# Kernel tuning notes

Measured on AMD Instinct MI355X. Metric: run time of the kernel, lower is better.

## Reference

```python
import jax, jax.numpy as jnp
import numpy as np

B, D, L, H = 8, 512, 2048, 8
DH = D // H
NEG = -1e30


def setup_inputs() -> dict:
    key = jax.random.key(0)
    k1, k2, k3, k4 = jax.random.split(key, 4)
    queries = jax.random.normal(k1, (B, D, L), dtype=jnp.float32)
    mask = jax.random.randint(k2, (B, L), 0, 2, dtype=jnp.int32)
    w_mem = jax.random.normal(k3, (2 * D, D), dtype=jnp.float32) * (1.0 / np.sqrt(D))
    w_q = jax.random.normal(k4, (D, D), dtype=jnp.float32) * (1.0 / np.sqrt(D))
    return {"queries": queries, "mask": mask, "w_mem": w_mem, "w_q": w_q}


def reference(queries, mask, w_mem, w_q):
    # 1x1 conv == pointwise GEMM over channel dim. queries: [B, D, L]
    memory = jnp.einsum('od,bdl->blo', w_mem, queries)  # [B, L, 2D]
    query = jnp.einsum('od,bdl->blo', w_q, queries)     # [B, L, D]

    def split_heads(x):  # [B, L, C] -> [B, H, L, C/H]
        b, l, c = x.shape
        return x.reshape(b, l, H, c // H).transpose(0, 2, 1, 3)

    k, v = memory[..., :D], memory[..., D:]
    Q = split_heads(query) * (DH ** -0.5)  # [B, H, L, DH]
    K = split_heads(k)
    V = split_heads(v)

    logits = jnp.einsum('bhqd,bhkd->bhqk', Q, K)  # [B, H, L, L]
    m = mask.astype(jnp.float32)[:, None, None, :]  # [B, 1, 1, L]
    logits = logits * m + (1.0 - m) * NEG
    weights = jax.nn.softmax(logits, axis=-1)
    x = jnp.einsum('bhqk,bhkd->bhqd', weights, V)  # [B, H, L, DH]
    # combine heads -> [B, L, D] -> transpose back to [B, D, L]
    out = x.transpose(0, 2, 1, 3).reshape(B, L, D).transpose(0, 2, 1)
    return out
```

## Files before the change

### kernel.cpp

```cpp
#include <hip/hip_runtime.h>
#include <hip/hip_bf16.h>

#define NB 8
#define ND 512
#define NL 2048
#define NH 8
#define NDH 64
#define VROWS 72

typedef __attribute__((ext_vector_type(8))) short bf16x8;
typedef __attribute__((ext_vector_type(4))) float f32x4;
typedef __attribute__((ext_vector_type(4))) unsigned int u32x4;

__device__ __forceinline__ unsigned short f2bf(float x) {
    return (unsigned short)((__float_as_uint(x) + 0x8000u) >> 16);
}

__device__ __forceinline__ float exp2_fast(float x) {
#if __has_builtin(__builtin_amdgcn_exp2f)
    return __builtin_amdgcn_exp2f(x);
#else
    return exp2f(x);
#endif
}

__device__ __forceinline__ unsigned int pack_bf16(float a, float b) {
    unsigned int ua = __float_as_uint(a) + 0x8000u;
    unsigned int ub = __float_as_uint(b) + 0x8000u;
    return __builtin_amdgcn_perm(ub, ua, 0x07060302u);
}

__device__ __forceinline__ void async16(void* lds, const void* g) {
    __builtin_amdgcn_global_load_lds(
        (const __attribute__((address_space(1))) unsigned int*)g,
        (__attribute__((address_space(3))) unsigned int*)lds, 16, 0, 0);
}

__global__ __launch_bounds__(256) void convert_w(
    const float* __restrict__ w_mem, const float* __restrict__ w_q,
    unsigned short* __restrict__ Wc)
{
    int idx = (blockIdx.x * 256 + threadIdx.x) * 8;
    int o = idx >> 9, k = idx & 511;
    const float* src;
    float sc;
    if (o < 1024) { src = w_mem + (size_t)o * ND + k; sc = 1.0f; }
    else          { src = w_q + (size_t)(o - 1024) * ND + k;
                    sc = 0.125f * 1.4426950408889634f; }
    float4 f0 = *(const float4*)src;
    float4 f1 = *(const float4*)(src + 4);
    ushort4 p0 = { f2bf(f0.x * sc), f2bf(f0.y * sc), f2bf(f0.z * sc), f2bf(f0.w * sc) };
    ushort4 p1 = { f2bf(f1.x * sc), f2bf(f1.y * sc), f2bf(f1.z * sc), f2bf(f1.w * sc) };
    *(ushort4*)(Wc + idx) = p0;
    *(ushort4*)(Wc + idx + 4) = p1;
}

__global__ __launch_bounds__(256) void convert_xt(
    const float* __restrict__ qin, unsigned short* __restrict__ Xt)
{
    __shared__ __align__(16) unsigned short T[64][72];
    const int b = blockIdx.z, d0 = blockIdx.y * 64, l0 = blockIdx.x * 64;
    const int t = threadIdx.x;
    const float* X = qin + ((size_t)b * ND + d0) * NL + l0;
    #pragma unroll
    for (int i = 0; i < 4; ++i) {
        int e = t + i * 256;
        int d = e >> 4, l4 = (e & 15) * 4;
        float4 v = *(const float4*)(X + (size_t)d * NL + l4);
        T[l4 + 0][d] = f2bf(v.x);
        T[l4 + 1][d] = f2bf(v.y);
        T[l4 + 2][d] = f2bf(v.z);
        T[l4 + 3][d] = f2bf(v.w);
    }
    __syncthreads();
    #pragma unroll
    for (int i = 0; i < 2; ++i) {
        int e = t + i * 256;
        int row = e >> 3, c8 = (e & 7) * 8;
        *(bf16x8*)(Xt + ((size_t)b * NL + l0 + row) * ND + d0 + c8) =
            *(const bf16x8*)&T[row][c8];
    }
}

__global__ __launch_bounds__(256) void write_vmask(
    const int* __restrict__ maskp, unsigned short* __restrict__ Vt)
{
    const int bh = blockIdx.x;
    const int b = bh >> 3;
    unsigned short* base = Vt + (size_t)bh * VROWS * NL;
    unsigned short* row64 = base + (size_t)64 * NL;
    for (int kk = threadIdx.x; kk < NL; kk += 256) {
        int s  = (kk & 32) | ((kk & 12) << 1) | ((kk & 16) >> 2) | (kk & 3);
        int lp = (kk & ~63) | s;
        row64[lp] = maskp[b * NL + kk] ? (unsigned short)0x3F80 : (unsigned short)0;
    }
    unsigned short* z = base + (size_t)65 * NL;
    for (int i = threadIdx.x; i < 7 * NL; i += 256) z[i] = 0;
}

__global__ __launch_bounds__(256, 3) void proj_mfma(
    const unsigned short* __restrict__ Wc,
    const unsigned short* __restrict__ Xt,
    const int* __restrict__ maskp,
    unsigned short* __restrict__ Kh,
    unsigned short* __restrict__ Qh,
    unsigned short* __restrict__ Vt)
{
    __shared__ __align__(16) unsigned short As[128 * 64];
    __shared__ __align__(16) unsigned short Bs[128 * 64];

    const int b  = blockIdx.z;
    const int m0 = blockIdx.y * 128;
    const int n0 = blockIdx.x * 128;
    const int t  = threadIdx.x;
    const int w = t >> 6, lane = t & 63, quad = lane >> 4, lq = lane & 15;
    const int wo = (w >> 1) * 64, wl = (w & 1) * 64;
    const int lr = lane >> 3;
    const int cbsw = (lane & 7) ^ lr;

    f32x4 acc[4][4];
    #pragma unroll
    for (int im = 0; im < 4; ++im)
        #pragma unroll
        for (int in = 0; in < 4; ++in)
            acc[im][in] = (f32x4){0.f, 0.f, 0.f, 0.f};

    for (int k0 = 0; k0 < ND; k0 += 64) {
        __syncthreads();
        #pragma unroll 2
        for (int i = w; i < 32; i += 4) {
            if (i < 16) {
                int R = i * 8;
                async16(&As[R * 64],
                        Wc + (size_t)(m0 + R + lr) * ND + k0 + cbsw * 8);
            } else {
                int R = (i - 16) * 8;
                async16(&Bs[R * 64],
                        Xt + ((size_t)b * NL + n0 + R + lr) * ND + k0 + cbsw * 8);
            }
        }
        __syncthreads();

        #pragma unroll
        for (int ks = 0; ks < 2; ++ks) {
            bf16x8 af[4], bfr[4];
            #pragma unroll
            for (int im = 0; im < 4; ++im) {
                int r = wo + im * 16 + lq;
                af[im] = *(const bf16x8*)&As[r * 64 + (((ks * 4 + quad) ^ (lq & 7)) * 8)];
            }
            #pragma unroll
            for (int in = 0; in < 4; ++in) {
                int r = wl + in * 16 + lq;
                bfr[in] = *(const bf16x8*)&Bs[r * 64 + (((ks * 4 + quad) ^ (lq & 7)) * 8)];
            }
            #pragma unroll
            for (int im = 0; im < 4; ++im)
                #pragma unroll
                for (int in = 0; in < 4; ++in)
                    acc[im][in] = __builtin_amdgcn_mfma_f32_16x16x32_bf16(
                        af[im], bfr[in], acc[im][in], 0, 0, 0);
        }
    }

    const int reg = (m0 + wo) >> 9;
    if (reg != 1) {
        unsigned short* dst = (reg == 0) ? Kh : Qh;
        #pragma unroll
        for (int im = 0; im < 4; ++im) {
            int o  = (m0 + wo + im * 16 + quad * 4) & 511;
            int hh = o >> 6, dh = o & 63;
            #pragma unroll
            for (int in = 0; in < 4; ++in) {
                int l = n0 + wl + in * 16 + lq;
                ushort4 pk = { f2bf(acc[im][in][0]), f2bf(acc[im][in][1]),
                               f2bf(acc[im][in][2]), f2bf(acc[im][in][3]) };
                *(ushort4*)&dst[(((size_t)b * NH + hh) * NL + l) * NDH + dh] = pk;
            }
        }
    } else {
        float mv[4];
        #pragma unroll
        for (int in = 0; in < 4; ++in)
            mv[in] = (float)maskp[b * NL + (n0 + wl + in * 16 + lq)];
        #pragma unroll
        for (int im = 0; im < 4; ++im) {
            int o  = (m0 + wo + im * 16 + quad * 4) & 511;
            int hh = o >> 6, dh = o & 63;
            #pragma unroll
            for (int in = 0; in < 4; ++in) {
                int l  = n0 + wl + in * 16 + lq;
                int kk = l & 63;
                int s  = (kk & 32) | ((kk & 12) << 1) | ((kk & 16) >> 2) | (kk & 3);
                int lp = (l & ~63) | s;
                #pragma unroll
                for (int r = 0; r < 4; ++r)
                    Vt[(((size_t)(b * NH + hh)) * VROWS + dh + r) * NL + lp] =
                        f2bf(acc[im][in][r] * mv[in]);
            }
        }
    }
}

__global__ __launch_bounds__(256, 2) void attn_mfma(
    const unsigned short* __restrict__ Qh,
    const unsigned short* __restrict__ Kh,
    const unsigned short* __restrict__ Vt,
    float* __restrict__ out)
{
    __shared__ __align__(16) unsigned short Ks2[2][64 * 64];
    __shared__ __align__(16) unsigned short Vs2[2][80 * 64];

    const int id = blockIdx.x;
    const int h  = id & 7;
    const int b  = (id >> 3) & 7;
    const int q0 = (id >> 6) * 256;
    const int t = threadIdx.x;
    const int w = t >> 6, lane = t & 63, quad = lane >> 4, lq = lane & 15;
    const int lr = lane >> 3;
    const int cbsw = (lane & 7) ^ lr;

    const unsigned short* Qg = Qh + ((size_t)(b * NH + h)) * NL * NDH;
    const unsigned short* Kg = Kh + ((size_t)(b * NH + h)) * NL * NDH;
    const unsigned short* Vg = Vt + ((size_t)(b * NH + h)) * VROWS * NL;

    #pragma unroll 2
    for (int i = w; i < 17; i += 4) {
        if (i < 8) {
            int R = i * 8;
            async16(&Ks2[0][R * 64], Kg + (size_t)(R + lr) * NDH + cbsw * 8);
        } else {
            int R = (i - 8) * 8;
            async16(&Vs2[0][R * 64], Vg + (size_t)(R + lr) * NL + cbsw * 8);
        }
    }

    bf16x8 qf[4][2];
    #pragma unroll
    for (int ni = 0; ni < 4; ++ni)
        #pragma unroll
        for (int ks = 0; ks < 2; ++ks)
            qf[ni][ks] = *(const bf16x8*)
                &Qg[(size_t)(q0 + w * 64 + ni * 16 + lq) * NDH + ks * 32 + quad * 8];

    f32x4 oacc[5][4];
    #pragma unroll
    for (int dm = 0; dm < 5; ++dm)
        #pragma unroll
        for (int ni = 0; ni < 4; ++ni)
            oacc[dm][ni] = (f32x4){0.f, 0.f, 0.f, 0.f};

    int cur = 0;
    for (int k0 = 0; k0 < NL; k0 += 64) {
        __syncthreads();

        if (k0 + 64 < NL) {
            const int kn = k0 + 64, nb = cur ^ 1;
            #pragma unroll 2
            for (int i = w; i < 17; i += 4) {
                if (i < 8) {
                    int R = i * 8;
                    async16(&Ks2[nb][R * 64],
                            Kg + (size_t)(kn + R + lr) * NDH + cbsw * 8);
                } else {
                    int R = (i - 8) * 8;
                    async16(&Vs2[nb][R * 64],
                            Vg + (size_t)(R + lr) * NL + kn + cbsw * 8);
                }
            }
        }

        const unsigned short* KsB = Ks2[cur];
        const unsigned short* VsB = Vs2[cur];

        f32x4 sacc[4][4];
        #pragma unroll
        for (int mi = 0; mi < 4; ++mi)
            #pragma unroll
            for (int ni = 0; ni < 4; ++ni)
                sacc[mi][ni] = (f32x4){0.f, 0.f, 0.f, 0.f};
        #pragma unroll
        for (int ks = 0; ks < 2; ++ks) {
            bf16x8 kf[4];
            #pragma unroll
            for (int mi = 0; mi < 4; ++mi)
                kf[mi] = *(const bf16x8*)
                    &KsB[(mi * 16 + lq) * 64 + (((ks * 4 + quad) ^ (lq & 7)) * 8)];
            #pragma unroll
            for (int mi = 0; mi < 4; ++mi)
                #pragma unroll
                for (int ni = 0; ni < 4; ++ni)
                    sacc[mi][ni] = __builtin_amdgcn_mfma_f32_16x16x32_bf16(
                        kf[mi], qf[ni][ks], sacc[mi][ni], 0, 0, 0);
        }

        u32x4 pfu[4][2];
        #pragma unroll
        for (int mi = 0; mi < 4; ++mi) {
            const int ks = mi >> 1, jp = (mi & 1) * 2;
            #pragma unroll
            for (int ni = 0; ni < 4; ++ni) {
                float e0 = exp2_fast(sacc[mi][ni][0]);
                float e1 = exp2_fast(sacc[mi][ni][1]);
                float e2 = exp2_fast(sacc[mi][ni][2]);
                float e3 = exp2_fast(sacc[mi][ni][3]);
                pfu[ni][ks][jp + 0] = pack_bf16(e0, e1);
                pfu[ni][ks][jp + 1] = pack_bf16(e2, e3);
            }
        }

        #pragma unroll
        for (int ks = 0; ks < 2; ++ks) {
            bf16x8 vf[5];
            #pragma unroll
            for (int dm = 0; dm < 5; ++dm)
                vf[dm] = *(const bf16x8*)
                    &VsB[(dm * 16 + lq) * 64 + (((ks * 4 + quad) ^ (lq & 7)) * 8)];
            #pragma unroll
            for (int dm = 0; dm < 5; ++dm)
                #pragma unroll
                for (int ni = 0; ni < 4; ++ni)
                    oacc[dm][ni] = __builtin_amdgcn_mfma_f32_16x16x32_bf16(
                        vf[dm], __builtin_bit_cast(bf16x8, pfu[ni][ks]),
                        oacc[dm][ni], 0, 0, 0);
        }
        cur ^= 1;
    }

    float inv[4];
    #pragma unroll
    for (int ni = 0; ni < 4; ++ni)
        inv[ni] = 1.0f / __shfl(oacc[4][ni][0], lq);

    #pragma unroll
    for (int dm = 0; dm < 4; ++dm)
        #pragma unroll
        for (int ni = 0; ni < 4; ++ni)
            #pragma unroll
            for (int r = 0; r < 4; ++r) {
                int dh = dm * 16 + quad * 4 + r;
                int l  = q0 + w * 64 + ni * 16 + lq;
                out[((size_t)b * ND + h * NDH + dh) * NL + l] =
                    oacc[dm][ni][r] * inv[ni];
            }
}

extern "C" void kernel_launch(void* const* d_in, const int* in_sizes, int n_in,
                              void* d_out, int out_size, void* d_ws, size_t ws_size,
                              hipStream_t stream) {
    const float* queries = (const float*)d_in[0];
    const int*   maskp   = (const int*)d_in[1];
    const float* w_mem   = (const float*)d_in[2];
    const float* w_q     = (const float*)d_in[3];
    float* out = (float*)d_out;

    const size_t headElems  = (size_t)NB * NH * NL * NDH;
    const size_t vElems     = (size_t)NB * NH * VROWS * NL;
    unsigned short* Kh = (unsigned short*)d_ws;
    unsigned short* Vt = Kh + headElems;
    unsigned short* Qh = Vt + vElems;
    unsigned short* Wc = Qh + headElems;
    unsigned short* Xt = Wc + (size_t)1536 * ND;

    convert_w<<<384, 256, 0, stream>>>(w_mem, w_q, Wc);

    dim3 gx(NL / 64, ND / 64, NB);
    convert_xt<<<gx, 256, 0, stream>>>(queries, Xt);

    write_vmask<<<NB * NH, 256, 0, stream>>>(maskp, Vt);

    dim3 g1(NL / 128, 1536 / 128, NB);
    proj_mfma<<<g1, 256, 0, stream>>>(Wc, Xt, maskp, Kh, Qh, Vt);

    attn_mfma<<<512, 256, 0, stream>>>(Qh, Kh, Vt, out);
}
```

Before: 204.6 us.

## Swap V-projection MFMA operands for vector stores, merge prep kernels, unroll attention loop

For the V rows of the projection, the MFMA operands are swapped so each lane holds four consecutive sequence positions. This lets the masked V tile be written with packed ushort4 stores, and the mask read as int4, instead of scattered 2-byte stores. The weight-conversion and V-mask-row kernels are merged into one launch, and the zeroing of the V padding rows 65-71 is dropped. The attention loop is unrolled by two with fixed double-buffer pointers, and the score accumulator starts from zero inside the first MFMA. The unzeroed padding rows feed MFMAs whose outputs are never stored, so correctness depends on that.

After: 225.0 us. +10.0%, slower.

```diff
diff --git a/kernel.cpp b/kernel.cpp
--- a/kernel.cpp
+++ b/kernel.cpp
@@ -36,23 +36,36 @@
         (__attribute__((address_space(3))) unsigned int*)lds, 16, 0, 0);
 }
 
-__global__ __launch_bounds__(256) void convert_w(
+__global__ __launch_bounds__(256) void prep_small(
     const float* __restrict__ w_mem, const float* __restrict__ w_q,
-    unsigned short* __restrict__ Wc)
+    const int* __restrict__ maskp,
+    unsigned short* __restrict__ Wc, unsigned short* __restrict__ Vt)
 {
-    int idx = (blockIdx.x * 256 + threadIdx.x) * 8;
-    int o = idx >> 9, k = idx & 511;
-    const float* src;
-    float sc;
-    if (o < 1024) { src = w_mem + (size_t)o * ND + k; sc = 1.0f; }
-    else          { src = w_q + (size_t)(o - 1024) * ND + k;
-                    sc = 0.125f * 1.4426950408889634f; }
-    float4 f0 = *(const float4*)src;
-    float4 f1 = *(const float4*)(src + 4);
-    ushort4 p0 = { f2bf(f0.x * sc), f2bf(f0.y * sc), f2bf(f0.z * sc), f2bf(f0.w * sc) };
-    ushort4 p1 = { f2bf(f1.x * sc), f2bf(f1.y * sc), f2bf(f1.z * sc), f2bf(f1.w * sc) };
-    *(ushort4*)(Wc + idx) = p0;
-    *(ushort4*)(Wc + idx + 4) = p1;
+    const int bid = blockIdx.x;
+    if (bid < 384) {
+        int idx = (bid * 256 + threadIdx.x) * 8;
+        int o = idx >> 9, k = idx & 511;
+        const float* src;
+        float sc;
+        if (o < 1024) { src = w_mem + (size_t)o * ND + k; sc = 1.0f; }
+        else          { src = w_q + (size_t)(o - 1024) * ND + k;
+                        sc = 0.125f * 1.4426950408889634f; }
+        float4 f0 = *(const float4*)src;
+        float4 f1 = *(const float4*)(src + 4);
+        ushort4 p0 = { f2bf(f0.x * sc), f2bf(f0.y * sc), f2bf(f0.z * sc), f2bf(f0.w * sc) };
+        ushort4 p1 = { f2bf(f1.x * sc), f2bf(f1.y * sc), f2bf(f1.z * sc), f2bf(f1.w * sc) };
+        *(ushort4*)(Wc + idx) = p0;
+        *(ushort4*)(Wc + idx + 4) = p1;
+    } else {
+        const int bh = bid - 384;
+        const int b = bh >> 3;
+        unsigned short* row64 = Vt + ((size_t)bh * VROWS + 64) * NL;
+        for (int kk = threadIdx.x; kk < NL; kk += 256) {
+            int s = (kk & 32) | ((kk & 12) << 1) | ((kk & 16) >> 2) | (kk & 3);
+            row64[(kk & ~63) | s] =
+                maskp[b * NL + kk] ? (unsigned short)0x3F80 : (unsigned short)0;
+        }
+    }
 }
 
 __global__ __launch_bounds__(256) void convert_xt(
@@ -80,22 +93,6 @@
         *(bf16x8*)(Xt + ((size_t)b * NL + l0 + row) * ND + d0 + c8) =
             *(const bf16x8*)&T[row][c8];
     }
-}
-
-__global__ __launch_bounds__(256) void write_vmask(
-    const int* __restrict__ maskp, unsigned short* __restrict__ Vt)
-{
-    const int bh = blockIdx.x;
-    const int b = bh >> 3;
-    unsigned short* base = Vt + (size_t)bh * VROWS * NL;
-    unsigned short* row64 = base + (size_t)64 * NL;
-    for (int kk = threadIdx.x; kk < NL; kk += 256) {
-        int s  = (kk & 32) | ((kk & 12) << 1) | ((kk & 16) >> 2) | (kk & 3);
-        int lp = (kk & ~63) | s;
-        row64[lp] = maskp[b * NL + kk] ? (unsigned short)0x3F80 : (unsigned short)0;
-    }
-    unsigned short* z = base + (size_t)65 * NL;
-    for (int i = threadIdx.x; i < 7 * NL; i += 256) z[i] = 0;
 }
 
 __global__ __launch_bounds__(256, 3) void proj_mfma(
@@ -117,13 +114,16 @@
     const int wo = (w >> 1) * 64, wl = (w & 1) * 64;
     const int lr = lane >> 3;
     const int cbsw = (lane & 7) ^ lr;
+    const bool isV = (m0 >= 512) && (m0 < 1024);
+    const f32x4 z4 = {0.f, 0.f, 0.f, 0.f};
 
     f32x4 acc[4][4];
     #pragma unroll
     for (int im = 0; im < 4; ++im)
         #pragma unroll
-        for (int in = 0; in < 4; ++in)
-            acc[im][in] = (f32x4){0.f, 0.f, 0.f, 0.f};
+        for (int in = 0; in < 4; ++in) acc[im][in] = z4;
+
+    const int sw[2] = {(quad ^ (lq & 7)) * 8, ((4 + quad) ^ (lq & 7)) * 8};
 
     for (int k0 = 0; k0 < ND; k0 += 64) {
         __syncthreads();
@@ -145,27 +145,31 @@
         for (int ks = 0; ks < 2; ++ks) {
             bf16x8 af[4], bfr[4];
             #pragma unroll
-            for (int im = 0; im < 4; ++im) {
-                int r = wo + im * 16 + lq;
-                af[im] = *(const bf16x8*)&As[r * 64 + (((ks * 4 + quad) ^ (lq & 7)) * 8)];
-            }
-            #pragma unroll
-            for (int in = 0; in < 4; ++in) {
-                int r = wl + in * 16 + lq;
-                bfr[in] = *(const bf16x8*)&Bs[r * 64 + (((ks * 4 + quad) ^ (lq & 7)) * 8)];
-            }
-            #pragma unroll
             for (int im = 0; im < 4; ++im)
-                #pragma unroll
-                for (int in = 0; in < 4; ++in)
-                    acc[im][in] = __builtin_amdgcn_mfma_f32_16x16x32_bf16(
-                        af[im], bfr[in], acc[im][in], 0, 0, 0);
-        }
-    }
-
-    const int reg = (m0 + wo) >> 9;
-    if (reg != 1) {
-        unsigned short* dst = (reg == 0) ? Kh : Qh;
+                af[im] = *(const bf16x8*)&As[(wo + im * 16 + lq) * 64 + sw[ks]];
+            #pragma unroll
+            for (int in = 0; in < 4; ++in)
+                bfr[in] = *(const bf16x8*)&Bs[(wl + in * 16 + lq) * 64 + sw[ks]];
+            if (!isV) {
+                #pragma unroll
+                for (int im = 0; im < 4; ++im)
+                    #pragma unroll
+                    for (int in = 0; in < 4; ++in)
+                        acc[im][in] = __builtin_amdgcn_mfma_f32_16x16x32_bf16(
+                            af[im], bfr[in], acc[im][in], 0, 0, 0);
+            } else {
+                #pragma unroll
+                for (int im = 0; im < 4; ++im)
+                    #pragma unroll
+                    for (int in = 0; in < 4; ++in)
+                        acc[im][in] = __builtin_amdgcn_mfma_f32_16x16x32_bf16(
+                            bfr[im], af[in], acc[im][in], 0, 0, 0);
+            }
+        }
+    }
+
+    if (!isV) {
+        unsigned short* dst = (m0 < 512) ? Kh : Qh;
         #pragma unroll
         for (int im = 0; im < 4; ++im) {
             int o  = (m0 + wo + im * 16 + quad * 4) & 511;
@@ -179,24 +183,23 @@
             }
         }
     } else {
-        float mv[4];
-        #pragma unroll
-        for (int in = 0; in < 4; ++in)
-            mv[in] = (float)maskp[b * NL + (n0 + wl + in * 16 + lq)];
         #pragma unroll
         for (int im = 0; im < 4; ++im) {
-            int o  = (m0 + wo + im * 16 + quad * 4) & 511;
-            int hh = o >> 6, dh = o & 63;
+            int l4 = n0 + wl + im * 16 + quad * 4;
+            int kk = l4 & 63;
+            int s4 = (kk & 32) | ((kk & 12) << 1) | ((kk & 16) >> 2);
+            int lp = (l4 & ~63) | s4;
+            int4 m4 = *(const int4*)&maskp[b * NL + l4];
+            float mv[4] = {(float)m4.x, (float)m4.y, (float)m4.z, (float)m4.w};
             #pragma unroll
             for (int in = 0; in < 4; ++in) {
-                int l  = n0 + wl + in * 16 + lq;
-                int kk = l & 63;
-                int s  = (kk & 32) | ((kk & 12) << 1) | ((kk & 16) >> 2) | (kk & 3);
-                int lp = (l & ~63) | s;
-                #pragma unroll
-                for (int r = 0; r < 4; ++r)
-                    Vt[(((size_t)(b * NH + hh)) * VROWS + dh + r) * NL + lp] =
-                        f2bf(acc[im][in][r] * mv[in]);
+                int o  = m0 - 512 + wo + in * 16 + lq;
+                int hh = o >> 6, dd = o & 63;
+                ushort4 pk = { f2bf(acc[im][in][0] * mv[0]),
+                               f2bf(acc[im][in][1] * mv[1]),
+                               f2bf(acc[im][in][2] * mv[2]),
+                               f2bf(acc[im][in][3] * mv[3]) };
+                *(ushort4*)&Vt[(((size_t)(b * NH + hh)) * VROWS + dd) * NL + lp] = pk;
             }
         }
     }
@@ -219,21 +222,28 @@
     const int w = t >> 6, lane = t & 63, quad = lane >> 4, lq = lane & 15;
     const int lr = lane >> 3;
     const int cbsw = (lane & 7) ^ lr;
+    const f32x4 z4 = {0.f, 0.f, 0.f, 0.f};
 
     const unsigned short* Qg = Qh + ((size_t)(b * NH + h)) * NL * NDH;
     const unsigned short* Kg = Kh + ((size_t)(b * NH + h)) * NL * NDH;
     const unsigned short* Vg = Vt + ((size_t)(b * NH + h)) * VROWS * NL;
 
-    #pragma unroll 2
-    for (int i = w; i < 17; i += 4) {
-        if (i < 8) {
-            int R = i * 8;
-            async16(&Ks2[0][R * 64], Kg + (size_t)(R + lr) * NDH + cbsw * 8);
-        } else {
-            int R = (i - 8) * 8;
-            async16(&Vs2[0][R * 64], Vg + (size_t)(R + lr) * NL + cbsw * 8);
-        }
-    }
+    const int sw[2] = {(quad ^ (lq & 7)) * 8, ((4 + quad) ^ (lq & 7)) * 8};
+
+    auto stage = [&](unsigned short* Kd, unsigned short* Vd, int kn) {
+        #pragma unroll 2
+        for (int i = w; i < 17; i += 4) {
+            if (i < 8) {
+                int R = i * 8;
+                async16(Kd + R * 64, Kg + (size_t)(kn + R + lr) * NDH + cbsw * 8);
+            } else {
+                int R = (i - 8) * 8;
+                async16(Vd + R * 64, Vg + (size_t)(R + lr) * NL + kn + cbsw * 8);
+            }
+        }
+    };
+
+    stage(Ks2[0], Vs2[0], 0);
 
     bf16x8 qf[4][2];
     #pragma unroll
@@ -247,51 +257,35 @@
     #pragma unroll
     for (int dm = 0; dm < 5; ++dm)
         #pragma unroll
-        for (int ni = 0; ni < 4; ++ni)
-            oacc[dm][ni] = (f32x4){0.f, 0.f, 0.f, 0.f};
-
-    int cur = 0;
-    for (int k0 = 0; k0 < NL; k0 += 64) {
+        for (int ni = 0; ni < 4; ++ni) oacc[dm][ni] = z4;
+
+    auto body = [&](const unsigned short* KsB, const unsigned short* VsB,
+                    unsigned short* KsN, unsigned short* VsN,
+                    int kn, bool pf) {
         __syncthreads();
-
-        if (k0 + 64 < NL) {
-            const int kn = k0 + 64, nb = cur ^ 1;
-            #pragma unroll 2
-            for (int i = w; i < 17; i += 4) {
-                if (i < 8) {
-                    int R = i * 8;
-                    async16(&Ks2[nb][R * 64],
-                            Kg + (size_t)(kn + R + lr) * NDH + cbsw * 8);
-                } else {
-                    int R = (i - 8) * 8;
-                    async16(&Vs2[nb][R * 64],
-                            Vg + (size_t)(R + lr) * NL + kn + cbsw * 8);
-                }
-            }
-        }
-
-        const unsigned short* KsB = Ks2[cur];
-        const unsigned short* VsB = Vs2[cur];
+        if (pf) stage(KsN, VsN, kn);
 
         f32x4 sacc[4][4];
-        #pragma unroll
-        for (int mi = 0; mi < 4; ++mi)
-            #pragma unroll
-            for (int ni = 0; ni < 4; ++ni)
-                sacc[mi][ni] = (f32x4){0.f, 0.f, 0.f, 0.f};
-        #pragma unroll
-        for (int ks = 0; ks < 2; ++ks) {
+        {
             bf16x8 kf[4];
             #pragma unroll
             for (int mi = 0; mi < 4; ++mi)
-                kf[mi] = *(const bf16x8*)
-                    &KsB[(mi * 16 + lq) * 64 + (((ks * 4 + quad) ^ (lq & 7)) * 8)];
+                kf[mi] = *(const bf16x8*)&KsB[(mi * 16 + lq) * 64 + sw[0]];
             #pragma unroll
             for (int mi = 0; mi < 4; ++mi)
                 #pragma unroll
                 for (int ni = 0; ni < 4; ++ni)
                     sacc[mi][ni] = __builtin_amdgcn_mfma_f32_16x16x32_bf16(
-                        kf[mi], qf[ni][ks], sacc[mi][ni], 0, 0, 0);
+                        kf[mi], qf[ni][0], z4, 0, 0, 0);
+            #pragma unroll
+            for (int mi = 0; mi < 4; ++mi)
+                kf[mi] = *(const bf16x8*)&KsB[(mi * 16 + lq) * 64 + sw[1]];
+            #pragma unroll
+            for (int mi = 0; mi < 4; ++mi)
+                #pragma unroll
+                for (int ni = 0; ni < 4; ++ni)
+                    sacc[mi][ni] = __builtin_amdgcn_mfma_f32_16x16x32_bf16(
+                        kf[mi], qf[ni][1], sacc[mi][ni], 0, 0, 0);
         }
 
         u32x4 pfu[4][2];
@@ -314,8 +308,7 @@
             bf16x8 vf[5];
             #pragma unroll
             for (int dm = 0; dm < 5; ++dm)
-                vf[dm] = *(const bf16x8*)
-                    &VsB[(dm * 16 + lq) * 64 + (((ks * 4 + quad) ^ (lq & 7)) * 8)];
+                vf[dm] = *(const bf16x8*)&VsB[(dm * 16 + lq) * 64 + sw[ks]];
             #pragma unroll
             for (int dm = 0; dm < 5; ++dm)
                 #pragma unroll
@@ -324,7 +317,11 @@
                         vf[dm], __builtin_bit_cast(bf16x8, pfu[ni][ks]),
                         oacc[dm][ni], 0, 0, 0);
         }
-        cur ^= 1;
+    };
+
+    for (int k0 = 0; k0 < NL; k0 += 128) {
+        body(Ks2[0], Vs2[0], Ks2[1], Vs2[1], k0 + 64, true);
+        body(Ks2[1], Vs2[1], Ks2[0], Vs2[0], k0 + 128, k0 + 128 < NL);
     }
 
     float inv[4];
@@ -362,13 +359,11 @@
     unsigned short* Wc = Qh + headElems;
     unsigned short* Xt = Wc + (size_t)1536 * ND;
 
-    convert_w<<<384, 256, 0, stream>>>(w_mem, w_q, Wc);
+    prep_small<<<448, 256, 0, stream>>>(w_mem, w_q, maskp, Wc, Vt);
 
     dim3 gx(NL / 64, ND / 64, NB);
     convert_xt<<<gx, 256, 0, stream>>>(queries, Xt);
 
-    write_vmask<<<NB * NH, 256, 0, stream>>>(maskp, Vt);
-
     dim3 g1(NL / 128, 1536 / 128, NB);
     proj_mfma<<<g1, 256, 0, stream>>>(Wc, Xt, maskp, Kh, Qh, Vt);
 
```
